# Kernel optimization log

Hardware: AMD Instinct MI355X
Metric: run time of the kernel (lower is better)

The kernel has to match this reference:

```python
import jax, jax.numpy as jnp
import numpy as np

B, S, E, H, F = 8, 1024, 1024, 16, 4096
D = E // H  # head_dim = 64
EPS = 1e-5


def setup_inputs() -> dict:
    key = jax.random.key(0)
    ks = jax.random.split(key, 12)
    s = 0.02
    return {
        "x": jax.random.normal(ks[0], (B, S, E), dtype=jnp.float32),
        # per-head projections (shared across heads), torch stores [out,in]; we use [in,out]
        "Wq": jax.random.normal(ks[1], (D, D), dtype=jnp.float32) * s,
        "Wk": jax.random.normal(ks[2], (D, D), dtype=jnp.float32) * s,
        "Wv": jax.random.normal(ks[3], (D, D), dtype=jnp.float32) * s,
        "Wo": jax.random.normal(ks[4], (E, E), dtype=jnp.float32) * s,
        "bo": jnp.zeros((E,), dtype=jnp.float32),
        "W1": jax.random.normal(ks[5], (E, F), dtype=jnp.float32) * s,
        "b1": jnp.zeros((F,), dtype=jnp.float32),
        "W2": jax.random.normal(ks[6], (F, E), dtype=jnp.float32) * s,
        "b2": jnp.zeros((E,), dtype=jnp.float32),
        "g1": jnp.ones((E,), dtype=jnp.float32),
        "beta1": jnp.zeros((E,), dtype=jnp.float32),
        "g2": jnp.ones((E,), dtype=jnp.float32),
        "beta2": jnp.zeros((E,), dtype=jnp.float32),
    }


def _layer_norm(x, g, b):
    m = jnp.mean(x, axis=-1, keepdims=True)
    v = jnp.mean(jnp.square(x - m), axis=-1, keepdims=True)
    return (x - m) * jax.lax.rsqrt(v + EPS) * g + b


def reference(x, Wq, Wk, Wv, Wo, bo, W1, b1, W2, b2, g1, beta1, g2, beta2):
    b, s, e = x.shape
    # --- attention sublayer (pre-norm) ---
    nx = _layer_norm(x, g1, beta1)
    h = nx.reshape(b, s, H, D)              # [B,S,H,D]
    q = h @ Wq                               # per-head linear, weight shared over heads
    k = h @ Wk
    v = h @ Wv
    energy = jnp.einsum('bqhd,bkhd->bhqk', q, k)  # full [B,H,S,S] scores
    mask = jnp.tril(jnp.ones((s, s), dtype=bool))
    energy = jnp.where(mask, energy, -jnp.inf)
    att = jax.nn.softmax(energy / jnp.sqrt(jnp.float32(e)), axis=-1)  # NOTE: scale by sqrt(embed_dim)
    o = jnp.einsum('bhqk,bkhd->bqhd', att, v).reshape(b, s, e)
    x = x + (o @ Wo + bo)
    # --- MLP sublayer (pre-norm); dropout is identity in eval ---
    nx = _layer_norm(x, g2, beta2)
    x = x + (jax.nn.relu(nx @ W1 + b1) @ W2 + b2)
    return x
```

## Files before the change

### kernel.cpp

```cpp
#include <hip/hip_runtime.h>

typedef unsigned short u16;
typedef __attribute__((ext_vector_type(4))) float f4;
typedef __attribute__((ext_vector_type(8))) short s8v;
typedef __attribute__((ext_vector_type(4))) unsigned short u16x4;

#define DEVINL __device__ __forceinline__

DEVINL float b2f(u16 u) { union { unsigned i; float f; } x; x.i = ((unsigned)u) << 16; return x.f; }
DEVINL u16 f2b(float f) {
  union { float f; unsigned i; } x; x.f = f;
  unsigned r = 0x7FFFu + ((x.i >> 16) & 1u);
  return (u16)((x.i + r) >> 16);
}

#define GLD_LDS16(g, l)                                                        \
  __builtin_amdgcn_global_load_lds((__attribute__((address_space(1))) void*)(g), \
                                   (__attribute__((address_space(3))) void*)(l), 16, 0, 0)

__global__ __launch_bounds__(256) void k_transpose(const float* __restrict__ in,
                                                   u16* __restrict__ out, int R, int C) {
  __shared__ float t[32][33];
  int tx = threadIdx.x & 31, ty = threadIdx.x >> 5;
  int c0 = blockIdx.x * 32, r0 = blockIdx.y * 32;
#pragma unroll
  for (int i = 0; i < 32; i += 8)
    t[ty + i][tx] = in[(long)(r0 + ty + i) * C + (c0 + tx)];
  __syncthreads();
#pragma unroll
  for (int i = 0; i < 32; i += 8)
    out[(long)(c0 + ty + i) * R + (r0 + tx)] = f2b(t[tx][ty + i]);
}

__global__ __launch_bounds__(256) void k_vtrans(const u16* __restrict__ v, u16* __restrict__ vt) {
  __shared__ u16 t[64][72];
  int bh = blockIdx.x, b = bh >> 4, h = bh & 15;
  int s0 = blockIdx.y * 64;
  int tid = threadIdx.x;
#pragma unroll
  for (int p = 0; p < 2; ++p) {
    int idx = p * 256 + tid;
    int sl = idx >> 3, c8 = (idx & 7) * 8;
    *(s8v*)(&t[sl][c8]) = *(const s8v*)(v + (((long)(b * 1024 + s0 + sl) * 16 + h) * 64) + c8);
  }
  __syncthreads();
#pragma unroll
  for (int p = 0; p < 2; ++p) {
    int idx = p * 256 + tid;
    int d = idx >> 3, c8 = (idx & 7) * 8;
    s8v o;
#pragma unroll
    for (int e = 0; e < 8; ++e) o[e] = (short)t[c8 + e][d];
    *(s8v*)(vt + ((long)bh * 64 + d) * 1024 + s0 + c8) = o;
  }
}

__global__ __launch_bounds__(256) void k_layernorm(const float* __restrict__ x,
                                                   const float* __restrict__ g,
                                                   const float* __restrict__ be,
                                                   u16* __restrict__ out) {
  long row = blockIdx.x;
  int tid = threadIdx.x;
  f4 v = ((const f4*)(x + row * 1024))[tid];
  float s = v[0] + v[1] + v[2] + v[3];
  float s2 = v[0] * v[0] + v[1] * v[1] + v[2] * v[2] + v[3] * v[3];
#pragma unroll
  for (int off = 32; off > 0; off >>= 1) {
    s += __shfl_down(s, off, 64);
    s2 += __shfl_down(s2, off, 64);
  }
  __shared__ float red[8];
  int wv = tid >> 6, ln = tid & 63;
  if (ln == 0) { red[wv] = s; red[4 + wv] = s2; }
  __syncthreads();
  s = red[0] + red[1] + red[2] + red[3];
  s2 = red[4] + red[5] + red[6] + red[7];
  float mean = s * (1.0f / 1024.0f);
  float var = s2 * (1.0f / 1024.0f) - mean * mean;
  float rs = rsqrtf(var + 1e-5f);
  f4 gg = ((const f4*)g)[tid];
  f4 bb = ((const f4*)be)[tid];
  u16x4 o;
#pragma unroll
  for (int i = 0; i < 4; ++i) o[i] = f2b((v[i] - mean) * rs * gg[i] + bb[i]);
  ((u16x4*)(out + row * 1024))[tid] = o;
}

__global__ __launch_bounds__(256) void k_qkv(const u16* __restrict__ nx, const u16* __restrict__ WqT,
                                             const u16* __restrict__ WkT, const u16* __restrict__ WvT,
                                             u16* __restrict__ q, u16* __restrict__ k,
                                             u16* __restrict__ v) {
  int tid = threadIdx.x, lane = tid & 63, wave = tid >> 6;
  int quad = lane >> 4, l16 = lane & 15;
  long rbase = (long)blockIdx.x * 64 + wave * 16;
  s8v a0 = *(const s8v*)(nx + (rbase + l16) * 64 + quad * 8);
  s8v a1 = *(const s8v*)(nx + (rbase + l16) * 64 + 32 + quad * 8);
  const u16* Ws[3] = {WqT, WkT, WvT};
  u16* Os[3] = {q, k, v};
#pragma unroll
  for (int t = 0; t < 3; ++t) {
#pragma unroll
    for (int j = 0; j < 4; ++j) {
      s8v b0 = *(const s8v*)(Ws[t] + (j * 16 + l16) * 64 + quad * 8);
      s8v b1 = *(const s8v*)(Ws[t] + (j * 16 + l16) * 64 + 32 + quad * 8);
      f4 acc = {0.f, 0.f, 0.f, 0.f};
      acc = __builtin_amdgcn_mfma_f32_16x16x32_bf16(a0, b0, acc, 0, 0, 0);
      acc = __builtin_amdgcn_mfma_f32_16x16x32_bf16(a1, b1, acc, 0, 0, 0);
#pragma unroll
      for (int r = 0; r < 4; ++r)
        Os[t][(rbase + quad * 4 + r) * 64 + j * 16 + l16] = f2b(acc[r]);
    }
  }
}

__global__ __launch_bounds__(256) void k_attn_mfma(const u16* __restrict__ q,
                                                   const u16* __restrict__ kk,
                                                   const u16* __restrict__ vt,
                                                   u16* __restrict__ o) {
  constexpr int LDK = 72;
  __shared__ u16 Ks[64 * LDK];
  __shared__ u16 Vt[64 * LDK];
  __shared__ u16 Ps[4][16 * LDK];
  int tid = threadIdx.x, lane = tid & 63, wave = tid >> 6;
  int quad = lane >> 4, l16 = lane & 15;
  int b = blockIdx.x >> 4, h = blockIdx.x & 15;
  int qi = (int)gridDim.y - 1 - (int)blockIdx.y;
  int q0 = qi * 64 + wave * 16;

  const u16* qp = q + (((long)(b * 1024 + q0 + l16)) * 16 + h) * 64;
  s8v aq0 = *(const s8v*)(qp + quad * 8);
  s8v aq1 = *(const s8v*)(qp + 32 + quad * 8);

  f4 O[4];
  float m_[4], l_[4];
#pragma unroll
  for (int jd = 0; jd < 4; ++jd) O[jd] = f4{0.f, 0.f, 0.f, 0.f};
#pragma unroll
  for (int r = 0; r < 4; ++r) { m_[r] = -__builtin_inff(); l_[r] = 0.f; }

  for (int kt = 0; kt <= qi; ++kt) {
    __syncthreads();
#pragma unroll
    for (int p = 0; p < 2; ++p) {
      int idx = p * 256 + tid;
      int row = idx >> 3, c8 = (idx & 7) * 8;
      *(s8v*)(Ks + row * LDK + c8) =
          *(const s8v*)(kk + (((long)(b * 1024 + kt * 64 + row)) * 16 + h) * 64 + c8);
      *(s8v*)(Vt + row * LDK + c8) =
          *(const s8v*)(vt + ((long)blockIdx.x * 64 + row) * 1024 + kt * 64 + c8);
    }
    __syncthreads();

    f4 sf[4];
#pragma unroll
    for (int jn = 0; jn < 4; ++jn) {
      s8v b0 = *(const s8v*)(Ks + (jn * 16 + l16) * LDK + quad * 8);
      s8v b1 = *(const s8v*)(Ks + (jn * 16 + l16) * LDK + 32 + quad * 8);
      f4 acc = f4{0.f, 0.f, 0.f, 0.f};
      acc = __builtin_amdgcn_mfma_f32_16x16x32_bf16(aq0, b0, acc, 0, 0, 0);
      acc = __builtin_amdgcn_mfma_f32_16x16x32_bf16(aq1, b1, acc, 0, 0, 0);
      sf[jn] = acc;
    }
    bool diag = (kt == qi);
    float rm[4];
#pragma unroll
    for (int r = 0; r < 4; ++r) rm[r] = -__builtin_inff();
#pragma unroll
    for (int jn = 0; jn < 4; ++jn)
#pragma unroll
      for (int r = 0; r < 4; ++r) {
        float v = sf[jn][r] * 0.03125f;
        if (diag && (jn * 16 + l16 > wave * 16 + quad * 4 + r)) v = -__builtin_inff();
        sf[jn][r] = v;
        rm[r] = fmaxf(rm[r], v);
      }
#pragma unroll
    for (int off = 1; off < 16; off <<= 1)
#pragma unroll
      for (int r = 0; r < 4; ++r) rm[r] = fmaxf(rm[r], __shfl_xor(rm[r], off, 64));
    float alpha[4], rs[4];
#pragma unroll
    for (int r = 0; r < 4; ++r) {
      float mn = fmaxf(m_[r], rm[r]);
      alpha[r] = __expf(m_[r] - mn);
      m_[r] = mn;
      rs[r] = 0.f;
    }
#pragma unroll
    for (int jn = 0; jn < 4; ++jn)
#pragma unroll
      for (int r = 0; r < 4; ++r) {
        float p = __expf(sf[jn][r] - m_[r]);
        rs[r] += p;
        Ps[wave][(quad * 4 + r) * LDK + jn * 16 + l16] = f2b(p);
      }
#pragma unroll
    for (int off = 1; off < 16; off <<= 1)
#pragma unroll
      for (int r = 0; r < 4; ++r) rs[r] += __shfl_xor(rs[r], off, 64);
#pragma unroll
    for (int r = 0; r < 4; ++r) l_[r] = l_[r] * alpha[r] + rs[r];
#pragma unroll
    for (int jd = 0; jd < 4; ++jd)
#pragma unroll
      for (int r = 0; r < 4; ++r) O[jd][r] *= alpha[r];
    asm volatile("s_waitcnt lgkmcnt(0)" ::: "memory");
    s8v p0 = *(const s8v*)(&Ps[wave][l16 * LDK + quad * 8]);
    s8v p1 = *(const s8v*)(&Ps[wave][l16 * LDK + 32 + quad * 8]);
#pragma unroll
    for (int jd = 0; jd < 4; ++jd) {
      s8v b0 = *(const s8v*)(Vt + (jd * 16 + l16) * LDK + quad * 8);
      s8v b1 = *(const s8v*)(Vt + (jd * 16 + l16) * LDK + 32 + quad * 8);
      O[jd] = __builtin_amdgcn_mfma_f32_16x16x32_bf16(p0, b0, O[jd], 0, 0, 0);
      O[jd] = __builtin_amdgcn_mfma_f32_16x16x32_bf16(p1, b1, O[jd], 0, 0, 0);
    }
  }
#pragma unroll
  for (int r = 0; r < 4; ++r) {
    float inv = 1.0f / l_[r];
    u16* op = o + (((long)(b * 1024 + q0 + quad * 4 + r)) * 16 + h) * 64;
#pragma unroll
    for (int jd = 0; jd < 4; ++jd) op[jd * 16 + l16] = f2b(O[jd][r] * inv);
  }
}

template <int EPI>
__global__ __launch_bounds__(256) void k_gemm_bt(const u16* __restrict__ A, const u16* __restrict__ BT,
                                                 const float* __restrict__ bias,
                                                 const float* __restrict__ resid,
                                                 void* __restrict__ outp, int M, int N, int K) {
  __shared__ u16 sA[3][128 * 32];
  __shared__ u16 sB[3][128 * 32];
  int tid = threadIdx.x, lane = tid & 63, wave = tid >> 6;
  int quad = lane >> 4, l16 = lane & 15;
  int wm = wave >> 1, wn = wave & 1;
  long bm = blockIdx.x, bn = blockIdx.y;
  int srow = tid >> 2, scol = (tid & 3) * 8;
  const u16* ga = A + (bm * 128 + srow) * (long)K + scol;
  const u16* gb = BT + (bn * 128 + srow) * (long)K + scol;
  int woff = wave * 1024;

  f4 acc[4][4];
#pragma unroll
  for (int i = 0; i < 4; ++i)
#pragma unroll
    for (int j = 0; j < 4; ++j) acc[i][j] = f4{0.f, 0.f, 0.f, 0.f};

#pragma unroll
  for (int t = 0; t < 2; ++t) {
    char* lA = (char*)&sA[t][0] + woff;
    char* lB = (char*)&sB[t][0] + woff;
    GLD_LDS16(ga + t * 32, lA);
    GLD_LDS16(ga + 64 * (long)K + t * 32, lA + 4096);
    GLD_LDS16(gb + t * 32, lB);
    GLD_LDS16(gb + 64 * (long)K + t * 32, lB + 4096);
  }

  int cur = 0;
  for (int k0 = 0; k0 < K; k0 += 32) {
    int k2 = k0 + 64;
    if (k2 < K) {
      asm volatile("s_waitcnt vmcnt(4)\n\ts_barrier" ::: "memory");
      int nb = cur >= 1 ? cur - 1 : 2;
      char* lA = (char*)&sA[nb][0] + woff;
      char* lB = (char*)&sB[nb][0] + woff;
      GLD_LDS16(ga + k2, lA);
      GLD_LDS16(ga + 64 * (long)K + k2, lA + 4096);
      GLD_LDS16(gb + k2, lB);
      GLD_LDS16(gb + 64 * (long)K + k2, lB + 4096);
    } else {
      asm volatile("s_waitcnt vmcnt(0)\n\ts_barrier" ::: "memory");
    }
    const u16* cA = sA[cur];
    const u16* cB = sB[cur];
    s8v aF[4], bF[4];
#pragma unroll
    for (int i = 0; i < 4; ++i)
      aF[i] = *(const s8v*)(cA + (wm * 64 + i * 16 + l16) * 32 + quad * 8);
#pragma unroll
    for (int j = 0; j < 4; ++j)
      bF[j] = *(const s8v*)(cB + (wn * 64 + j * 16 + l16) * 32 + quad * 8);
#pragma unroll
    for (int i = 0; i < 4; ++i)
#pragma unroll
      for (int j = 0; j < 4; ++j)
        acc[i][j] = __builtin_amdgcn_mfma_f32_16x16x32_bf16(aF[i], bF[j], acc[i][j], 0, 0, 0);
    cur = cur < 2 ? cur + 1 : 0;
  }

#pragma unroll
  for (int i = 0; i < 4; ++i) {
#pragma unroll
    for (int j = 0; j < 4; ++j) {
      long row = bm * 128 + wm * 64 + i * 16 + quad * 4;
      int col = (int)bn * 128 + wn * 64 + j * 16 + l16;
      float bcol = bias[col];
#pragma unroll
      for (int r = 0; r < 4; ++r) {
        float val = acc[i][j][r] + bcol;
        if (EPI == 1) {
          ((u16*)outp)[(row + r) * (long)N + col] = f2b(val > 0.f ? val : 0.f);
        } else {
          ((float*)outp)[(row + r) * (long)N + col] = resid[(row + r) * (long)N + col] + val;
        }
      }
    }
  }
}

template <int EPI>
__global__ __launch_bounds__(512) void k_gemm256(const u16* __restrict__ A,
                                                 const u16* __restrict__ BT,
                                                 const float* __restrict__ bias,
                                                 const float* __restrict__ resid,
                                                 void* __restrict__ outp, int M, int N, int K) {
  __shared__ __align__(16) u16 S[65536];
  int tid = threadIdx.x, lane = tid & 63, wave = tid >> 6;
  int l16 = lane & 15, quad = lane >> 4;
  int wm = wave >> 2, wn = wave & 3;
  long bm = blockIdx.x, bn = blockIdx.y;

  int swx = ((l16 >> 3) & 1) << 4;
  int baseA = (((wm * 64 + l16) * 32) + quad * 8) ^ swx;
  int baseB = (((wn * 32 + l16) * 32) + quad * 8) ^ swx;

  int Lb = tid * 16;
  int Ls = Lb ^ (((Lb >> 9) & 1) << 5);
  int r_ = Ls >> 6, kin = (Ls & 63) >> 1;
  const u16* pA = A + (bm * 256 + r_) * (long)K + kin;
  const u16* pB = BT + (bn * 256 + r_) * (long)K + kin;

  f4 acc[4][4][2];
#pragma unroll
  for (int q = 0; q < 4; ++q)
#pragma unroll
    for (int mi = 0; mi < 4; ++mi)
#pragma unroll
      for (int nj = 0; nj < 2; ++nj) acc[q][mi][nj] = f4{0.f, 0.f, 0.f, 0.f};
  s8v aF[4][2], bF[2][2][2];

#define BAR asm volatile("s_barrier" ::: "memory")
#define LGK0 asm volatile("s_waitcnt lgkmcnt(0)" ::: "memory")
#define WVM4 asm volatile("s_waitcnt vmcnt(4)" ::: "memory")
#define WVM0 asm volatile("s_waitcnt vmcnt(0)" ::: "memory")

#define STAGE(mat, half, t, buf)                                               \
  do {                                                                         \
    const u16* g_ = ((mat) ? pB : pA) + (long)(half) * 128 * K + (t) * 64;     \
    char* l_ = ((char*)S) + ((buf) * 32768 + (mat) * 16384 + (half) * 8192) * 2 + wave * 1024; \
    GLD_LDS16(g_, l_);                                                         \
    GLD_LDS16(g_ + 32, l_ + 8192);                                             \
  } while (0)

#define LDA(buf, mh)                                                           \
  do {                                                                         \
    const u16* p_ = S + (buf) * 32768 + (mh) * 8192 + baseA;                   \
    _Pragma("unroll") for (int mi = 0; mi < 4; ++mi) {                         \
      aF[mi][0] = *(const s8v*)(p_ + mi * 512);                                \
      aF[mi][1] = *(const s8v*)(p_ + mi * 512 + 4096);                         \
    }                                                                          \
  } while (0)

#define LDB(buf, nh, set)                                                      \
  do {                                                                         \
    const u16* p_ = S + (buf) * 32768 + 16384 + (nh) * 8192 + baseB;           \
    _Pragma("unroll") for (int nj = 0; nj < 2; ++nj) {                         \
      bF[set][nj][0] = *(const s8v*)(p_ + nj * 512);                           \
      bF[set][nj][1] = *(const s8v*)(p_ + nj * 512 + 4096);                    \
    }                                                                          \
  } while (0)

#define MM(q)                                                                  \
  do {                                                                         \
    _Pragma("unroll") for (int mi = 0; mi < 4; ++mi)                           \
        _Pragma("unroll") for (int nj = 0; nj < 2; ++nj) {                     \
      acc[q][mi][nj] = __builtin_amdgcn_mfma_f32_16x16x32_bf16(                \
          aF[mi][0], bF[(q) & 1][nj][0], acc[q][mi][nj], 0, 0, 0);             \
      acc[q][mi][nj] = __builtin_amdgcn_mfma_f32_16x16x32_bf16(                \
          aF[mi][1], bF[(q) & 1][nj][1], acc[q][mi][nj], 0, 0, 0);             \
    }                                                                          \
  } while (0)

#define PHASES(t, LAST)                                                        \
                                             \
  LDA(0, 0); LDB(0, 0, 0); STAGE(0, 1, (t) + 1, 1);                            \
  BAR; LGK0; __builtin_amdgcn_s_setprio(1); MM(0); __builtin_amdgcn_s_setprio(0); BAR; \
                                                           \
  LDB(0, 1, 1); STAGE(1, 1, (t) + 1, 1);                                       \
  BAR; LGK0; __builtin_amdgcn_s_setprio(1); MM(1); __builtin_amdgcn_s_setprio(0); BAR; \
                                                           \
  LDA(0, 1); if (!(LAST)) STAGE(0, 0, (t) + 2, 0);                             \
  BAR; LGK0; __builtin_amdgcn_s_setprio(1); MM(2); __builtin_amdgcn_s_setprio(0); BAR; \
                                          \
  if (!(LAST)) STAGE(1, 0, (t) + 2, 0);                                        \
  __builtin_amdgcn_s_setprio(1); MM(3); __builtin_amdgcn_s_setprio(0);         \
  if (LAST) { WVM0; } else { WVM4; }                                           \
  BAR;                                                                         \
                                           \
  LDA(1, 0); LDB(1, 0, 0); if (!(LAST)) STAGE(0, 1, (t) + 2, 0);               \
  BAR; LGK0; __builtin_amdgcn_s_setprio(1); MM(0); __builtin_amdgcn_s_setprio(0); BAR; \
                                                           \
  LDB(1, 1, 1); if (!(LAST)) STAGE(1, 1, (t) + 2, 0);                          \
  BAR; LGK0; __builtin_amdgcn_s_setprio(1); MM(1); __builtin_amdgcn_s_setprio(0); BAR; \
                                                           \
  LDA(1, 1); if (!(LAST)) STAGE(0, 0, (t) + 3, 1);                             \
  BAR; LGK0; __builtin_amdgcn_s_setprio(1); MM(2); __builtin_amdgcn_s_setprio(0); BAR; \
                                                           \
  if (!(LAST)) STAGE(1, 0, (t) + 3, 1);                                        \
  __builtin_amdgcn_s_setprio(1); MM(3); __builtin_amdgcn_s_setprio(0);         \
  if (!(LAST)) { WVM4; BAR; }

  STAGE(0, 0, 0, 0);
  STAGE(1, 0, 0, 0);
  STAGE(0, 1, 0, 0);
  STAGE(1, 1, 0, 0);
  STAGE(0, 0, 1, 1);
  STAGE(1, 0, 1, 1);
  WVM4; BAR;

  int NI = K >> 7;
  for (int i = 0; i < NI - 1; ++i) {
    int t = 2 * i;
    PHASES(t, 0);
  }
  {
    int t = 2 * (NI - 1);
    PHASES(t, 1);
  }

#undef PHASES
#undef MM
#undef LDB
#undef LDA
#undef STAGE
#undef WVM0
#undef WVM4
#undef LGK0
#undef BAR

#pragma unroll
  for (int q = 0; q < 4; ++q) {
    int mh = q >> 1, nh = q & 1;
#pragma unroll
    for (int mi = 0; mi < 4; ++mi) {
#pragma unroll
      for (int nj = 0; nj < 2; ++nj) {
        long row = bm * 256 + mh * 128 + wm * 64 + mi * 16 + quad * 4;
        int col = (int)bn * 256 + nh * 128 + wn * 32 + nj * 16 + l16;
        float bcol = bias[col];
#pragma unroll
        for (int rr = 0; rr < 4; ++rr) {
          float val = acc[q][mi][nj][rr] + bcol;
          if (EPI == 1) {
            ((u16*)outp)[(row + rr) * (long)N + col] = f2b(val > 0.f ? val : 0.f);
          } else {
            ((float*)outp)[(row + rr) * (long)N + col] =
                resid[(row + rr) * (long)N + col] + val;
          }
        }
      }
    }
  }
}

extern "C" void kernel_launch(void* const* d_in, const int* in_sizes, int n_in, void* d_out,
                              int out_size, void* d_ws, size_t ws_size, hipStream_t stream) {
  const float* x = (const float*)d_in[0];
  const float* Wq = (const float*)d_in[1];
  const float* Wk = (const float*)d_in[2];
  const float* Wv = (const float*)d_in[3];
  const float* Wo = (const float*)d_in[4];
  const float* bo = (const float*)d_in[5];
  const float* W1 = (const float*)d_in[6];
  const float* b1 = (const float*)d_in[7];
  const float* W2 = (const float*)d_in[8];
  const float* b2 = (const float*)d_in[9];
  const float* g1 = (const float*)d_in[10];
  const float* be1 = (const float*)d_in[11];
  const float* g2 = (const float*)d_in[12];
  const float* be2 = (const float*)d_in[13];

  char* ws = (char*)d_ws;
  const size_t MB = 1ull << 20;
  u16* nx = (u16*)(ws + 0);
  u16* qb = (u16*)(ws + 16 * MB);
  u16* kb = (u16*)(ws + 32 * MB);
  u16* vb = (u16*)(ws + 48 * MB);
  float* x1 = (float*)(ws + 64 * MB);
  u16* h1 = (u16*)(ws + 96 * MB);
  u16* vtr = (u16*)(ws + 96 * MB);
  u16* WoT = (u16*)(ws + 160 * MB);
  u16* W1T = (u16*)(ws + 162 * MB);
  u16* W2T = (u16*)(ws + 170 * MB);
  u16* WqT = (u16*)(ws + 178 * MB);
  u16* WkT = WqT + 64 * 64;
  u16* WvT = WkT + 64 * 64;
  u16* ob = nx;
  u16* nx2 = qb;

  k_transpose<<<dim3(32, 32), 256, 0, stream>>>(Wo, WoT, 1024, 1024);
  k_transpose<<<dim3(128, 32), 256, 0, stream>>>(W1, W1T, 1024, 4096);
  k_transpose<<<dim3(32, 128), 256, 0, stream>>>(W2, W2T, 4096, 1024);
  k_transpose<<<dim3(2, 2), 256, 0, stream>>>(Wq, WqT, 64, 64);
  k_transpose<<<dim3(2, 2), 256, 0, stream>>>(Wk, WkT, 64, 64);
  k_transpose<<<dim3(2, 2), 256, 0, stream>>>(Wv, WvT, 64, 64);

  k_layernorm<<<8192, 256, 0, stream>>>(x, g1, be1, nx);
  k_qkv<<<2048, 256, 0, stream>>>(nx, WqT, WkT, WvT, qb, kb, vb);
  k_vtrans<<<dim3(128, 16), 256, 0, stream>>>(vb, vtr);
  k_attn_mfma<<<dim3(128, 16), 256, 0, stream>>>(qb, kb, vtr, ob);
  k_gemm_bt<2><<<dim3(64, 8), 256, 0, stream>>>(ob, WoT, bo, x, x1, 8192, 1024, 1024);

  k_layernorm<<<8192, 256, 0, stream>>>(x1, g2, be2, nx2);
  k_gemm256<1><<<dim3(32, 16), 512, 0, stream>>>(nx2, W1T, b1, nullptr, h1, 8192, 4096, 1024);
  k_gemm_bt<2><<<dim3(64, 8), 256, 0, stream>>>(h1, W2T, b2, x1, d_out, 8192, 1024, 4096);
}
```

Measured before the change: 448.0 us.

## Run W2 GEMM on 256-tile kernel with split-K and combine pass

The second MLP GEMM moves from the smaller-tile k_gemm_bt kernel to the 256x256 k_gemm256 kernel. K is split in two across blockIdx.z so the 32x4 tile grid gets 256 blocks. The LDS staging layout changes to 64-wide K rows with a different swizzle, and a leading-dimension parameter is added. Partial sums go to fp32 workspace and a new combine kernel adds them with bias and residual. This costs extra global traffic for two 32MB partial buffers plus one more launch, in exchange for better per-block MFMA efficiency and occupancy.

New measurement: 436.7 us. 2.5% less time.

```diff
diff --git a/kernel.cpp b/kernel.cpp
--- a/kernel.cpp
+++ b/kernel.cpp
@@ -313,22 +313,25 @@
                                                  const u16* __restrict__ BT,
                                                  const float* __restrict__ bias,
                                                  const float* __restrict__ resid,
-                                                 void* __restrict__ outp, int M, int N, int K) {
+                                                 void* __restrict__ outp, int M, int N, int K,
+                                                 int lda) {
   __shared__ __align__(16) u16 S[65536];
   int tid = threadIdx.x, lane = tid & 63, wave = tid >> 6;
   int l16 = lane & 15, quad = lane >> 4;
   int wm = wave >> 2, wn = wave & 3;
   long bm = blockIdx.x, bn = blockIdx.y;
-
-  int swx = ((l16 >> 3) & 1) << 4;
-  int baseA = (((wm * 64 + l16) * 32) + quad * 8) ^ swx;
-  int baseB = (((wn * 32 + l16) * 32) + quad * 8) ^ swx;
+  int z = blockIdx.z;
+
+  int swx = ((l16 >> 2) & 1) << 4;
+  int colsw = (quad * 8) ^ swx;
+  int baseA = (wm * 64 + l16) * 64 + colsw;
+  int baseB = (wn * 32 + l16) * 64 + colsw;
 
   int Lb = tid * 16;
   int Ls = Lb ^ (((Lb >> 9) & 1) << 5);
-  int r_ = Ls >> 6, kin = (Ls & 63) >> 1;
-  const u16* pA = A + (bm * 256 + r_) * (long)K + kin;
-  const u16* pB = BT + (bn * 256 + r_) * (long)K + kin;
+  int r_ = Ls >> 7, kin = (Ls & 127) >> 1;
+  const u16* pA = A + (bm * 256 + r_) * (long)lda + kin + (long)z * K;
+  const u16* pB = BT + (bn * 256 + r_) * (long)lda + kin + (long)z * K;
 
   f4 acc[4][4][2];
 #pragma unroll
@@ -346,18 +349,18 @@
 
 #define STAGE(mat, half, t, buf)                                               \
   do {                                                                         \
-    const u16* g_ = ((mat) ? pB : pA) + (long)(half) * 128 * K + (t) * 64;     \
+    const u16* g_ = ((mat) ? pB : pA) + (long)(half) * 128 * lda + (t) * 64;   \
     char* l_ = ((char*)S) + ((buf) * 32768 + (mat) * 16384 + (half) * 8192) * 2 + wave * 1024; \
     GLD_LDS16(g_, l_);                                                         \
-    GLD_LDS16(g_ + 32, l_ + 8192);                                             \
+    GLD_LDS16(g_ + 64 * (long)lda, l_ + 8192);                                 \
   } while (0)
 
 #define LDA(buf, mh)                                                           \
   do {                                                                         \
     const u16* p_ = S + (buf) * 32768 + (mh) * 8192 + baseA;                   \
     _Pragma("unroll") for (int mi = 0; mi < 4; ++mi) {                         \
-      aF[mi][0] = *(const s8v*)(p_ + mi * 512);                                \
-      aF[mi][1] = *(const s8v*)(p_ + mi * 512 + 4096);                         \
+      aF[mi][0] = *(const s8v*)(p_ + mi * 1024);                               \
+      aF[mi][1] = *(const s8v*)(p_ + mi * 1024 + 32);                          \
     }                                                                          \
   } while (0)
 
@@ -365,8 +368,8 @@
   do {                                                                         \
     const u16* p_ = S + (buf) * 32768 + 16384 + (nh) * 8192 + baseB;           \
     _Pragma("unroll") for (int nj = 0; nj < 2; ++nj) {                         \
-      bF[set][nj][0] = *(const s8v*)(p_ + nj * 512);                           \
-      bF[set][nj][1] = *(const s8v*)(p_ + nj * 512 + 4096);                    \
+      bF[set][nj][0] = *(const s8v*)(p_ + nj * 1024);                          \
+      bF[set][nj][1] = *(const s8v*)(p_ + nj * 1024 + 32);                     \
     }                                                                          \
   } while (0)
 
@@ -438,6 +441,7 @@
 #undef LGK0
 #undef BAR
 
+  float* P0 = (EPI == 0) ? ((float*)outp + (long)z * M * N) : nullptr;
 #pragma unroll
   for (int q = 0; q < 4; ++q) {
     int mh = q >> 1, nh = q & 1;
@@ -447,11 +451,14 @@
       for (int nj = 0; nj < 2; ++nj) {
         long row = bm * 256 + mh * 128 + wm * 64 + mi * 16 + quad * 4;
         int col = (int)bn * 256 + nh * 128 + wn * 32 + nj * 16 + l16;
-        float bcol = bias[col];
+        float bcol = 0.f;
+        if (EPI != 0) bcol = bias[col];
 #pragma unroll
         for (int rr = 0; rr < 4; ++rr) {
           float val = acc[q][mi][nj][rr] + bcol;
-          if (EPI == 1) {
+          if (EPI == 0) {
+            P0[(row + rr) * (long)N + col] = val;
+          } else if (EPI == 1) {
             ((u16*)outp)[(row + rr) * (long)N + col] = f2b(val > 0.f ? val : 0.f);
           } else {
             ((float*)outp)[(row + rr) * (long)N + col] =
@@ -460,6 +467,21 @@
         }
       }
     }
+  }
+}
+
+__global__ __launch_bounds__(256) void k_combine(const float* __restrict__ P,
+                                                 const float* __restrict__ resid,
+                                                 const float* __restrict__ bias,
+                                                 float* __restrict__ out) {
+  const f4* P0 = (const f4*)P;
+  const f4* P1 = P0 + 2097152;
+  const f4* R = (const f4*)resid;
+  const f4* Bv = (const f4*)bias;
+  f4* O = (f4*)out;
+  for (int i = blockIdx.x * 256 + threadIdx.x; i < 2097152; i += 2048 * 256) {
+    f4 a = P0[i], b = P1[i], r = R[i], bb = Bv[i & 255];
+    O[i] = a + b + r + bb;
   }
 }
 
@@ -497,6 +519,7 @@
   u16* WvT = WkT + 64 * 64;
   u16* ob = nx;
   u16* nx2 = qb;
+  float* Pk = (float*)ws;
 
   k_transpose<<<dim3(32, 32), 256, 0, stream>>>(Wo, WoT, 1024, 1024);
   k_transpose<<<dim3(128, 32), 256, 0, stream>>>(W1, W1T, 1024, 4096);
@@ -512,6 +535,7 @@
   k_gemm_bt<2><<<dim3(64, 8), 256, 0, stream>>>(ob, WoT, bo, x, x1, 8192, 1024, 1024);
 
   k_layernorm<<<8192, 256, 0, stream>>>(x1, g2, be2, nx2);
-  k_gemm256<1><<<dim3(32, 16), 512, 0, stream>>>(nx2, W1T, b1, nullptr, h1, 8192, 4096, 1024);
-  k_gemm_bt<2><<<dim3(64, 8), 256, 0, stream>>>(h1, W2T, b2, x1, d_out, 8192, 1024, 4096);
-}
+  k_gemm256<1><<<dim3(32, 16, 1), 512, 0, stream>>>(nx2, W1T, b1, nullptr, h1, 8192, 4096, 1024, 1024);
+  k_gemm256<0><<<dim3(32, 4, 2), 512, 0, stream>>>(h1, W2T, nullptr, nullptr, Pk, 8192, 1024, 2048, 4096);
+  k_combine<<<2048, 256, 0, stream>>>(Pk, x1, b2, (float*)d_out);
+}
```
